# Kernel tuning notes

Measured on AMD Instinct MI355X. Metric: run time of the kernel, lower is better.

Reference implementation:

```python
import jax, jax.numpy as jnp
import numpy as np

DIM = 180
HEADS = 6
HEAD_DIM = DIM // HEADS
SCALE = HEAD_DIM ** (-0.5)
BW, N, K = 8192, 64, 16


def setup_inputs() -> dict:
    key = jax.random.key(0)
    ks = jax.random.split(key, 6)
    return {
        "x": jax.random.normal(ks[0], (BW, N, DIM), dtype=jnp.float32),
        "bpe_windows": jax.random.normal(ks[1], (BW, N, K), dtype=jnp.float32),
        "qkv_w": jax.random.normal(ks[2], (3 * DIM, DIM), dtype=jnp.float32) * 0.05,
        "qkv_b": jax.random.normal(ks[3], (3 * DIM,), dtype=jnp.float32) * 0.05,
        "proj_w": jax.random.normal(ks[4], (DIM, DIM), dtype=jnp.float32) * 0.05,
        "proj_b": jax.random.normal(ks[5], (DIM,), dtype=jnp.float32) * 0.05,
        "tau": jnp.ones((HEADS, 1, 1), dtype=jnp.float32),
    }


def reference(x, bpe_windows, qkv_w, qkv_b, proj_w, proj_b, tau):
    B_, n, C = x.shape
    # qkv projection -> (3, B_, H, N, hd)
    qkv = (x @ qkv_w.T + qkv_b).reshape(B_, n, 3, HEADS, HEAD_DIM)
    qkv = jnp.transpose(qkv, (2, 0, 3, 1, 4))
    q, k, v = qkv[0], qkv[1], qkv[2]
    q = q * SCALE
    attn = jnp.einsum("bhid,bhjd->bhij", q, k)  # (B_, H, N, N)
    # geodesic bias from BPE embeddings: d_B(i,j) = ||bpe_i - bpe_j||_2
    diff = bpe_windows[:, :, None, :] - bpe_windows[:, None, :, :]  # (B_, N, N, K)
    d_B = jnp.sqrt(jnp.sum(diff * diff, axis=-1))  # (B_, N, N)
    log_W_geo = -d_B[:, None, :, :] / jnp.clip(tau, 1e-6)[None]  # (B_, H, N, N)
    attn = jax.nn.softmax(attn + log_W_geo, axis=-1)
    out = jnp.einsum("bhij,bhjd->bhid", attn, v)  # (B_, H, N, hd)
    out = jnp.transpose(out, (0, 2, 1, 3)).reshape(B_, n, C)
    return out @ proj_w.T + proj_b
```

## Files before the change

kernel.cpp:

```cpp
#include <hip/hip_runtime.h>
#include <hip/hip_fp16.h>
#include <hip/hip_bf16.h>
#include <math.h>

typedef __attribute__((ext_vector_type(8))) short short8b;
typedef __attribute__((ext_vector_type(4))) float f32x4;
typedef __attribute__((ext_vector_type(4))) unsigned short ushort4b;

#define NWIN 8192
#define NT   512
#define SCALE 0.18257418583505536f

#define XB_P 200
#define QK_P 200
#define VT_P 72
#define DB_P 68
#define ATT_P 184

#define OFF_XB  0
#define OFF_QK  25600
#define OFF_VT  51200
#define OFF_DB  65024
#define OFF_BPE 73728
#define LDS_BYTES 78848

#define WK 192

__device__ __forceinline__ unsigned int bf2pk(float lo, float hi) {
    union { __hip_bfloat162 h; unsigned int u; } cv;
    cv.h = __float22bfloat162_rn(make_float2(lo, hi));
    return cv.u;
}
__device__ __forceinline__ unsigned short bf1(float v) {
    union { __hip_bfloat16 h; unsigned short u; } cv;
    cv.h = __float2bfloat16(v);
    return cv.u;
}

__global__ void prep_weights(const float* __restrict__ qkv_w,
                             const float* __restrict__ proj_w,
                             unsigned short* __restrict__ wqr,
                             unsigned short* __restrict__ wpr)
{
    const int idx = blockIdx.x * 256 + threadIdx.x;
    if (idx < 540 * WK) {
        const int r = idx / WK, k = idx % WK;
        const int seg = r / 30, dd = r % 30;
        const int which = seg / 6, hh = seg % 6;
        float v = 0.f;
        if (k < 180)
            v = qkv_w[(which * 180 + hh * 30 + dd) * 180 + k];
        wqr[idx] = bf1(v);
    }
    const int j = idx - 540 * WK;
    if (j >= 0 && j < WK * WK) {
        const int r = j / WK, k = j % WK;
        float v = 0.f;
        if (r < 180 && k < 180)
            v = proj_w[r * 180 + k];
        wpr[j] = bf1(v);
    }
}

__global__ void __launch_bounds__(NT, 3)
waga_mfma(const float* __restrict__ x,
          const float* __restrict__ bpe,
          const unsigned short* __restrict__ wqr,
          const unsigned short* __restrict__ wpr,
          const float* __restrict__ qkv_b,
          const float* __restrict__ proj_b,
          const float* __restrict__ tau,
          float* __restrict__ out)
{
    extern __shared__ char smem[];
    unsigned short* xb   = (unsigned short*)(smem + OFF_XB);
    unsigned short* qk   = (unsigned short*)(smem + OFF_QK);
    unsigned short* vT   = (unsigned short*)(smem + OFF_VT);
    unsigned short* dBs  = (unsigned short*)(smem + OFF_DB);
    float*          bpes = (float*)(smem + OFF_BPE);

    const int b = blockIdx.x;
    const int t = threadIdx.x;
    const int w = t >> 6;
    const int l = t & 63;
    const int lr = l & 15;
    const int g  = l >> 4;

    unsigned short* attg = (unsigned short*)((char*)out + (size_t)b * 46080 + 22528);

    if (t < 192) {
        const int n = t / 3, c = t % 3;
        *reinterpret_cast<uint2*>(xb + n * XB_P + 180 + 4 * c) = make_uint2(0u, 0u);
    } else if (t < 256) {
        const int n = t - 192;
        ushort4b z = {0, 0, 0, 0};
        *reinterpret_cast<ushort4b*>(attg + n * ATT_P + 180) = z;
    }
    {
        const float* xw = x + (size_t)b * 11520;
        for (int i = t; i < 64 * 45; i += NT) {
            const int n = i / 45, c4 = i % 45;
            const float4 v = *reinterpret_cast<const float4*>(xw + i * 4);
            *reinterpret_cast<uint2*>(xb + n * XB_P + c4 * 4) =
                make_uint2(bf2pk(v.x, v.y), bf2pk(v.z, v.w));
        }
    }
    if (t < 256) {
        const float4 v = *reinterpret_cast<const float4*>(bpe + (size_t)b * 1024 + t * 4);
        *reinterpret_cast<float4*>(bpes + (t >> 2) * 20 + (t & 3) * 4) = v;
    }
    __syncthreads();

    {
        const int ti = t >> 4, tj = t & 15;
        float acc0[4] = {0.f, 0.f, 0.f, 0.f};
        float acc1[4] = {0.f, 0.f, 0.f, 0.f};
        #pragma unroll
        for (int k4 = 0; k4 < 4; ++k4) {
            const float4 a0 = *reinterpret_cast<const float4*>(bpes + ti * 20 + 4 * k4);
            const float4 a1 = *reinterpret_cast<const float4*>(bpes + (ti + 32) * 20 + 4 * k4);
            #pragma unroll
            for (int e = 0; e < 4; ++e) {
                const float4 bb = *reinterpret_cast<const float4*>(bpes + (tj + 16 * e) * 20 + 4 * k4);
                float d;
                d = a0.x - bb.x; acc0[e] += d * d;
                d = a0.y - bb.y; acc0[e] += d * d;
                d = a0.z - bb.z; acc0[e] += d * d;
                d = a0.w - bb.w; acc0[e] += d * d;
                d = a1.x - bb.x; acc1[e] += d * d;
                d = a1.y - bb.y; acc1[e] += d * d;
                d = a1.z - bb.z; acc1[e] += d * d;
                d = a1.w - bb.w; acc1[e] += d * d;
            }
        }
        #pragma unroll
        for (int e = 0; e < 4; ++e) {
            dBs[ti * DB_P + tj + 16 * e] =
                __half_as_ushort(__float2half_rn(sqrtf(acc0[e])));
            dBs[(ti + 32) * DB_P + tj + 16 * e] =
                __half_as_ushort(__float2half_rn(sqrtf(acc1[e])));
        }
    }

    for (int pass = 0; pass < 2; ++pass) {
        if (pass) __syncthreads();

        {
            f32x4 acc[3][4];
            const unsigned short* wrow[3];
            bool has[3], arow_ok[3];
            int whichv[3], hhl[3], halfv[3];
            #pragma unroll
            for (int ti = 0; ti < 3; ++ti) {
                const int tl = w + 8 * ti;
                has[ti] = (tl < 18);
                const int tls = has[ti] ? tl : 0;
                const int segl = tls >> 1;
                halfv[ti] = tls & 1;
                whichv[ti] = segl / 3;
                hhl[ti] = segl % 3;
                const int hg = 3 * pass + hhl[ti];
                const int wseg = whichv[ti] * 6 + hg;
                const int ddr = halfv[ti] * 16 + lr;
                arow_ok[ti] = (ddr < 30);
                wrow[ti] = wqr + (size_t)(wseg * 30 + (arow_ok[ti] ? ddr : 0)) * WK;
                const int ddb = halfv[ti] * 16 + g * 4;
                const int cbase = whichv[ti] * 180 + hg * 30;
                f32x4 binit;
                #pragma unroll
                for (int i = 0; i < 4; ++i)
                    binit[i] = (ddb + i < 30) ? qkv_b[cbase + ddb + i] : 0.f;
                #pragma unroll
                for (int mt = 0; mt < 4; ++mt) acc[ti][mt] = binit;
            }
            #pragma unroll
            for (int kk = 0; kk < 6; ++kk) {
                short8b xf[4];
                #pragma unroll
                for (int mt = 0; mt < 4; ++mt)
                    xf[mt] = *reinterpret_cast<const short8b*>(
                        xb + (mt * 16 + lr) * XB_P + kk * 32 + g * 8);
                #pragma unroll
                for (int ti = 0; ti < 3; ++ti) {
                    if (!has[ti]) continue;
                    short8b wfv;
                    if (arow_ok[ti])
                        wfv = *reinterpret_cast<const short8b*>(wrow[ti] + kk * 32 + g * 8);
                    else
                        wfv = short8b{0, 0, 0, 0, 0, 0, 0, 0};
                    #pragma unroll
                    for (int mt = 0; mt < 4; ++mt)
                        acc[ti][mt] = __builtin_amdgcn_mfma_f32_16x16x32_bf16(
                            wfv, xf[mt], acc[ti][mt], 0, 0, 0);
                }
            }
            #pragma unroll
            for (int ti = 0; ti < 3; ++ti) {
                if (!has[ti]) continue;
                const int ddb = halfv[ti] * 16 + g * 4;
                #pragma unroll
                for (int mt = 0; mt < 4; ++mt) {
                    const int tok = mt * 16 + lr;
                    float v0 = acc[ti][mt][0], v1 = acc[ti][mt][1];
                    float v2 = acc[ti][mt][2], v3 = acc[ti][mt][3];
                    if (whichv[ti] == 0) { v0 *= SCALE; v1 *= SCALE; v2 *= SCALE; v3 *= SCALE; }
                    if (whichv[ti] < 2) {
                        *reinterpret_cast<uint2*>(
                            qk + tok * QK_P + hhl[ti] * 64 + whichv[ti] * 32 + ddb) =
                            make_uint2(bf2pk(v0, v1), bf2pk(v2, v3));
                    } else {
                        const int c = (tok & 32) + ((tok >> 2) & 3) * 8 + ((tok >> 4) & 1) * 4 + (tok & 3);
                        unsigned short* vb = vT + hhl[ti] * 2304 + ddb * VT_P + c;
                        vb[0 * VT_P] = bf1(v0);
                        vb[1 * VT_P] = bf1(v1);
                        vb[2 * VT_P] = bf1(v2);
                        vb[3 * VT_P] = bf1(v3);
                    }
                }
            }
        }
        __syncthreads();

        for (int u = w; u < 12; u += 8) {
            const int hh = u >> 2, mt = u & 3;
            const int h = 3 * pass + hh;
            const int tok = mt * 16 + lr;
            const unsigned short* qkh = qk + hh * 64;
            const short8b qf = *reinterpret_cast<const short8b*>(
                qkh + tok * QK_P + g * 8);
            short8b kf[4];
            #pragma unroll
            for (int jt = 0; jt < 4; ++jt)
                kf[jt] = *reinterpret_cast<const short8b*>(
                    qkh + (jt * 16 + lr) * QK_P + 32 + g * 8);
            short8b vf[2][2];
            #pragma unroll
            for (int ntd = 0; ntd < 2; ++ntd)
                #pragma unroll
                for (int ks = 0; ks < 2; ++ks)
                    vf[ntd][ks] = *reinterpret_cast<const short8b*>(
                        vT + hh * 2304 + (ntd * 16 + lr) * VT_P + ks * 32 + g * 8);
            const float itau = 1.f / fmaxf(tau[h], 1e-6f);
            f32x4 s[4];
            #pragma unroll
            for (int jt = 0; jt < 4; ++jt) {
                const ushort4b du = *reinterpret_cast<const ushort4b*>(
                    dBs + tok * DB_P + jt * 16 + g * 4);
                #pragma unroll
                for (int i = 0; i < 4; ++i)
                    s[jt][i] = -itau * __half2float(__ushort_as_half(du[i]));
            }
            __builtin_amdgcn_s_setprio(1);
            #pragma unroll
            for (int jt = 0; jt < 4; ++jt)
                s[jt] = __builtin_amdgcn_mfma_f32_16x16x32_bf16(kf[jt], qf, s[jt], 0, 0, 0);
            __builtin_amdgcn_s_setprio(0);
            float m4[4], a4[4];
            #pragma unroll
            for (int i = 0; i < 4; ++i)
                m4[i] = fmaxf(fmaxf(s[0][i], s[1][i]), fmaxf(s[2][i], s[3][i]));
            float mx = fmaxf(fmaxf(m4[0], m4[1]), fmaxf(m4[2], m4[3]));
            mx = fmaxf(mx, __shfl_xor(mx, 16));
            mx = fmaxf(mx, __shfl_xor(mx, 32));
            #pragma unroll
            for (int jt = 0; jt < 4; ++jt)
                #pragma unroll
                for (int i = 0; i < 4; ++i)
                    s[jt][i] = __expf(s[jt][i] - mx);
            #pragma unroll
            for (int i = 0; i < 4; ++i)
                a4[i] = (s[0][i] + s[1][i]) + (s[2][i] + s[3][i]);
            float sum = (a4[0] + a4[1]) + (a4[2] + a4[3]);
            sum += __shfl_xor(sum, 16);
            sum += __shfl_xor(sum, 32);
            const float inv = 1.f / sum;
            union { short8b v; unsigned int u[4]; } pb[2];
            #pragma unroll
            for (int ks = 0; ks < 2; ++ks) {
                pb[ks].u[0] = bf2pk(s[2 * ks][0] * inv, s[2 * ks][1] * inv);
                pb[ks].u[1] = bf2pk(s[2 * ks][2] * inv, s[2 * ks][3] * inv);
                pb[ks].u[2] = bf2pk(s[2 * ks + 1][0] * inv, s[2 * ks + 1][1] * inv);
                pb[ks].u[3] = bf2pk(s[2 * ks + 1][2] * inv, s[2 * ks + 1][3] * inv);
            }
            __builtin_amdgcn_s_setprio(1);
            f32x4 o0 = {0.f, 0.f, 0.f, 0.f}, o1 = {0.f, 0.f, 0.f, 0.f};
            o0 = __builtin_amdgcn_mfma_f32_16x16x32_bf16(vf[0][0], pb[0].v, o0, 0, 0, 0);
            o1 = __builtin_amdgcn_mfma_f32_16x16x32_bf16(vf[1][0], pb[0].v, o1, 0, 0, 0);
            o0 = __builtin_amdgcn_mfma_f32_16x16x32_bf16(vf[0][1], pb[1].v, o0, 0, 0, 0);
            o1 = __builtin_amdgcn_mfma_f32_16x16x32_bf16(vf[1][1], pb[1].v, o1, 0, 0, 0);
            __builtin_amdgcn_s_setprio(0);
            {
                const int col0 = h * 30 + g * 4;
                *reinterpret_cast<uint2*>(attg + tok * ATT_P + col0) =
                    make_uint2(bf2pk(o0[0], o0[1]), bf2pk(o0[2], o0[3]));
                const int col1 = h * 30 + 16 + g * 4;
                if (g < 3) {
                    *reinterpret_cast<uint2*>(attg + tok * ATT_P + col1) =
                        make_uint2(bf2pk(o1[0], o1[1]), bf2pk(o1[2], o1[3]));
                } else {
                    *reinterpret_cast<unsigned int*>(attg + tok * ATT_P + col1) =
                        bf2pk(o1[0], o1[1]);
                }
            }
        }
    }
    __syncthreads();

    {
        const int mt = w & 3;
        const int ntb = (w >> 2) * 6;
        short8b attf[6];
        #pragma unroll
        for (int kk = 0; kk < 6; ++kk) {
            if (kk == 5 && g == 3)
                attf[kk] = short8b{0, 0, 0, 0, 0, 0, 0, 0};
            else
                attf[kk] = *reinterpret_cast<const short8b*>(
                    attg + (mt * 16 + lr) * ATT_P + kk * 32 + g * 8);
        }
        f32x4 pacc[6];
        short8b wf[6];
        #pragma unroll
        for (int kk = 0; kk < 6; ++kk)
            wf[kk] = *reinterpret_cast<const short8b*>(
                wpr + (size_t)(ntb * 16 + lr) * WK + kk * 32 + g * 8);
        #pragma unroll
        for (int q6 = 0; q6 < 6; ++q6) {
            short8b wcur[6];
            #pragma unroll
            for (int kk = 0; kk < 6; ++kk) wcur[kk] = wf[kk];
            if (q6 < 5) {
                const unsigned short* wrown =
                    wpr + (size_t)((ntb + q6 + 1) * 16 + lr) * WK;
                #pragma unroll
                for (int kk = 0; kk < 6; ++kk)
                    wf[kk] = *reinterpret_cast<const short8b*>(wrown + kk * 32 + g * 8);
            }
            const int cb = (ntb + q6) * 16 + g * 4;
            f32x4 acc;
            #pragma unroll
            for (int i = 0; i < 4; ++i)
                acc[i] = (cb + i < 180) ? proj_b[cb + i] : 0.f;
            #pragma unroll
            for (int kk = 0; kk < 6; ++kk)
                acc = __builtin_amdgcn_mfma_f32_16x16x32_bf16(wcur[kk], attf[kk], acc, 0, 0, 0);
            pacc[q6] = acc;
        }
        __syncthreads();
        #pragma unroll
        for (int q6 = 0; q6 < 6; ++q6) {
            const int cb = (ntb + q6) * 16 + g * 4;
            if (cb < 177) {
                const int tok = mt * 16 + lr;
                *reinterpret_cast<float4*>(out + ((size_t)b * 64 + tok) * 180 + cb) =
                    make_float4(pacc[q6][0], pacc[q6][1], pacc[q6][2], pacc[q6][3]);
            }
        }
    }
}

extern "C" void kernel_launch(void* const* d_in, const int* in_sizes, int n_in,
                              void* d_out, int out_size, void* d_ws, size_t ws_size,
                              hipStream_t stream) {
    (void)in_sizes; (void)n_in; (void)out_size; (void)ws_size;
    const float* x      = (const float*)d_in[0];
    const float* bpe    = (const float*)d_in[1];
    const float* qkv_w  = (const float*)d_in[2];
    const float* qkv_b  = (const float*)d_in[3];
    const float* proj_w = (const float*)d_in[4];
    const float* proj_b = (const float*)d_in[5];
    const float* tau    = (const float*)d_in[6];

    unsigned short* wqr = (unsigned short*)d_ws;
    unsigned short* wpr = wqr + 540 * WK;

    prep_weights<<<(540 * WK + WK * WK + 255) / 256, 256, 0, stream>>>(
        qkv_w, proj_w, wqr, wpr);

    (void)hipFuncSetAttribute((const void*)waga_mfma,
                              hipFuncAttributeMaxDynamicSharedMemorySize,
                              LDS_BYTES);
    waga_mfma<<<NWIN, NT, LDS_BYTES, stream>>>(x, bpe, wqr, wpr, qkv_b, proj_b, tau,
                                               (float*)d_out);
}
```

Before: 737.0 us.

## Switch QKV and output projections to 32x32x16 bf16 MFMA tiles

Rewrites the QKV projection and the output projection to use 32x32x16 bf16 MFMA instructions in place of 16x16x32 ones. Each wave now covers a 32-token by 32-channel tile, and the work is split across waves differently. The QKV bias moves into LDS and is added after accumulation instead of seeding the accumulators. The aim is fewer MFMA issues and fewer fragment loads per output element, at the cost of larger accumulator register use and a different output index mapping, which could pressure occupancy.

```diff
diff --git a/kernel.cpp b/kernel.cpp
--- a/kernel.cpp
+++ b/kernel.cpp
@@ -5,6 +5,7 @@
 
 typedef __attribute__((ext_vector_type(8))) short short8b;
 typedef __attribute__((ext_vector_type(4))) float f32x4;
+typedef __attribute__((ext_vector_type(16))) float f32x16;
 typedef __attribute__((ext_vector_type(4))) unsigned short ushort4b;
 
 #define NWIN 8192
@@ -17,12 +18,13 @@
 #define DB_P 68
 #define ATT_P 184
 
-#define OFF_XB  0
-#define OFF_QK  25600
-#define OFF_VT  51200
-#define OFF_DB  65024
-#define OFF_BPE 73728
-#define LDS_BYTES 78848
+#define OFF_XB   0
+#define OFF_QK   25600
+#define OFF_VT   51200
+#define OFF_DB   65024
+#define OFF_BPE  73728
+#define OFF_QKVB 78848
+#define LDS_BYTES 81152
 
 #define WK 192
 
@@ -78,6 +80,7 @@
     unsigned short* vT   = (unsigned short*)(smem + OFF_VT);
     unsigned short* dBs  = (unsigned short*)(smem + OFF_DB);
     float*          bpes = (float*)(smem + OFF_BPE);
+    float*          qkvb = (float*)(smem + OFF_QKVB);
 
     const int b = blockIdx.x;
     const int t = threadIdx.x;
@@ -85,6 +88,8 @@
     const int l = t & 63;
     const int lr = l & 15;
     const int g  = l >> 4;
+    const int r31 = l & 31;
+    const int h5 = l >> 5;
 
     unsigned short* attg = (unsigned short*)((char*)out + (size_t)b * 46080 + 22528);
 
@@ -108,6 +113,11 @@
     if (t < 256) {
         const float4 v = *reinterpret_cast<const float4*>(bpe + (size_t)b * 1024 + t * 4);
         *reinterpret_cast<float4*>(bpes + (t >> 2) * 20 + (t & 3) * 4) = v;
+    }
+    for (int i = t; i < 576; i += NT) {
+        const int segp = i >> 5, dd = i & 31;
+        const int which = segp / 6, hg = segp % 6;
+        qkvb[i] = (dd < 30) ? qkv_b[which * 180 + hg * 30 + dd] : 0.f;
     }
     __syncthreads();
 
@@ -146,71 +156,58 @@
         if (pass) __syncthreads();
 
         {
-            f32x4 acc[3][4];
-            const unsigned short* wrow[3];
-            bool has[3], arow_ok[3];
-            int whichv[3], hhl[3], halfv[3];
-            #pragma unroll
-            for (int ti = 0; ti < 3; ++ti) {
-                const int tl = w + 8 * ti;
-                has[ti] = (tl < 18);
-                const int tls = has[ti] ? tl : 0;
-                const int segl = tls >> 1;
-                halfv[ti] = tls & 1;
-                whichv[ti] = segl / 3;
-                hhl[ti] = segl % 3;
-                const int hg = 3 * pass + hhl[ti];
-                const int wseg = whichv[ti] * 6 + hg;
-                const int ddr = halfv[ti] * 16 + lr;
-                arow_ok[ti] = (ddr < 30);
-                wrow[ti] = wqr + (size_t)(wseg * 30 + (arow_ok[ti] ? ddr : 0)) * WK;
-                const int ddb = halfv[ti] * 16 + g * 4;
-                const int cbase = whichv[ti] * 180 + hg * 30;
-                f32x4 binit;
-                #pragma unroll
-                for (int i = 0; i < 4; ++i)
-                    binit[i] = (ddb + i < 30) ? qkv_b[cbase + ddb + i] : 0.f;
-                #pragma unroll
-                for (int mt = 0; mt < 4; ++mt) acc[ti][mt] = binit;
-            }
-            #pragma unroll
-            for (int kk = 0; kk < 6; ++kk) {
-                short8b xf[4];
-                #pragma unroll
-                for (int mt = 0; mt < 4; ++mt)
-                    xf[mt] = *reinterpret_cast<const short8b*>(
-                        xb + (mt * 16 + lr) * XB_P + kk * 32 + g * 8);
-                #pragma unroll
-                for (int ti = 0; ti < 3; ++ti) {
-                    if (!has[ti]) continue;
-                    short8b wfv;
-                    if (arow_ok[ti])
-                        wfv = *reinterpret_cast<const short8b*>(wrow[ti] + kk * 32 + g * 8);
-                    else
-                        wfv = short8b{0, 0, 0, 0, 0, 0, 0, 0};
-                    #pragma unroll
-                    for (int mt = 0; mt < 4; ++mt)
-                        acc[ti][mt] = __builtin_amdgcn_mfma_f32_16x16x32_bf16(
-                            wfv, xf[mt], acc[ti][mt], 0, 0, 0);
+            const int tt = w & 1;
+            const bool has2 = (w < 2);
+            const bool aok = (r31 < 30);
+            const unsigned short* xrow = xb + (tt * 32 + r31) * XB_P;
+            int segp[3], which_[3], hh_[3];
+            const unsigned short* arow[3];
+            #pragma unroll
+            for (int i = 0; i < 3; ++i) {
+                const int tl = (w + 8 * i < 18) ? (w + 8 * i) : w;
+                const int seg = tl >> 1;
+                which_[i] = seg / 3; hh_[i] = seg % 3;
+                segp[i] = which_[i] * 6 + 3 * pass + hh_[i];
+                arow[i] = wqr + (size_t)(segp[i] * 30 + (aok ? r31 : 0)) * WK;
+            }
+            f32x16 acc[3];
+            #pragma unroll
+            for (int i = 0; i < 3; ++i)
+                #pragma unroll
+                for (int j = 0; j < 16; ++j) acc[i][j] = 0.f;
+            const short8b zf = {0, 0, 0, 0, 0, 0, 0, 0};
+            #pragma unroll
+            for (int kk = 0; kk < 12; ++kk) {
+                const short8b bfv = *reinterpret_cast<const short8b*>(xrow + kk * 16 + h5 * 8);
+                const short8b a0 = aok ? *reinterpret_cast<const short8b*>(arow[0] + kk * 16 + h5 * 8) : zf;
+                acc[0] = __builtin_amdgcn_mfma_f32_32x32x16_bf16(a0, bfv, acc[0], 0, 0, 0);
+                const short8b a1 = aok ? *reinterpret_cast<const short8b*>(arow[1] + kk * 16 + h5 * 8) : zf;
+                acc[1] = __builtin_amdgcn_mfma_f32_32x32x16_bf16(a1, bfv, acc[1], 0, 0, 0);
+                if (has2) {
+                    const short8b a2 = aok ? *reinterpret_cast<const short8b*>(arow[2] + kk * 16 + h5 * 8) : zf;
+                    acc[2] = __builtin_amdgcn_mfma_f32_32x32x16_bf16(a2, bfv, acc[2], 0, 0, 0);
                 }
             }
-            #pragma unroll
-            for (int ti = 0; ti < 3; ++ti) {
-                if (!has[ti]) continue;
-                const int ddb = halfv[ti] * 16 + g * 4;
-                #pragma unroll
-                for (int mt = 0; mt < 4; ++mt) {
-                    const int tok = mt * 16 + lr;
-                    float v0 = acc[ti][mt][0], v1 = acc[ti][mt][1];
-                    float v2 = acc[ti][mt][2], v3 = acc[ti][mt][3];
-                    if (whichv[ti] == 0) { v0 *= SCALE; v1 *= SCALE; v2 *= SCALE; v3 *= SCALE; }
-                    if (whichv[ti] < 2) {
-                        *reinterpret_cast<uint2*>(
-                            qk + tok * QK_P + hhl[ti] * 64 + whichv[ti] * 32 + ddb) =
+            const int tok = tt * 32 + r31;
+            const int cperm = (tok & 32) + ((tok >> 2) & 3) * 8 + ((tok >> 4) & 1) * 4 + (tok & 3);
+            #pragma unroll
+            for (int i = 0; i < 3; ++i) {
+                if (i == 2 && !has2) continue;
+                const int wq_ = which_[i], hhv = hh_[i];
+                #pragma unroll
+                for (int q = 0; q < 4; ++q) {
+                    const int db = 8 * q + 4 * h5;
+                    const float4 bias = *reinterpret_cast<const float4*>(qkvb + segp[i] * 32 + db);
+                    float v0 = acc[i][4 * q + 0] + bias.x;
+                    float v1 = acc[i][4 * q + 1] + bias.y;
+                    float v2 = acc[i][4 * q + 2] + bias.z;
+                    float v3 = acc[i][4 * q + 3] + bias.w;
+                    if (wq_ == 0) { v0 *= SCALE; v1 *= SCALE; v2 *= SCALE; v3 *= SCALE; }
+                    if (wq_ < 2) {
+                        *reinterpret_cast<uint2*>(qk + tok * QK_P + hhv * 64 + wq_ * 32 + db) =
                             make_uint2(bf2pk(v0, v1), bf2pk(v2, v3));
                     } else {
-                        const int c = (tok & 32) + ((tok >> 2) & 3) * 8 + ((tok >> 4) & 1) * 4 + (tok & 3);
-                        unsigned short* vb = vT + hhl[ti] * 2304 + ddb * VT_P + c;
+                        unsigned short* vb = vT + hhv * 2304 + db * VT_P + cperm;
                         vb[0 * VT_P] = bf1(v0);
                         vb[1 * VT_P] = bf1(v1);
                         vb[2 * VT_P] = bf1(v2);
@@ -307,53 +304,51 @@
     __syncthreads();
 
     {
-        const int mt = w & 3;
-        const int ntb = (w >> 2) * 6;
-        short8b attf[6];
-        #pragma unroll
-        for (int kk = 0; kk < 6; ++kk) {
-            if (kk == 5 && g == 3)
-                attf[kk] = short8b{0, 0, 0, 0, 0, 0, 0, 0};
-            else
-                attf[kk] = *reinterpret_cast<const short8b*>(
-                    attg + (mt * 16 + lr) * ATT_P + kk * 32 + g * 8);
-        }
-        f32x4 pacc[6];
-        short8b wf[6];
-        #pragma unroll
-        for (int kk = 0; kk < 6; ++kk)
-            wf[kk] = *reinterpret_cast<const short8b*>(
-                wpr + (size_t)(ntb * 16 + lr) * WK + kk * 32 + g * 8);
-        #pragma unroll
-        for (int q6 = 0; q6 < 6; ++q6) {
-            short8b wcur[6];
-            #pragma unroll
-            for (int kk = 0; kk < 6; ++kk) wcur[kk] = wf[kk];
-            if (q6 < 5) {
-                const unsigned short* wrown =
-                    wpr + (size_t)((ntb + q6 + 1) * 16 + lr) * WK;
-                #pragma unroll
-                for (int kk = 0; kk < 6; ++kk)
-                    wf[kk] = *reinterpret_cast<const short8b*>(wrown + kk * 32 + g * 8);
-            }
-            const int cb = (ntb + q6) * 16 + g * 4;
-            f32x4 acc;
-            #pragma unroll
-            for (int i = 0; i < 4; ++i)
-                acc[i] = (cb + i < 180) ? proj_b[cb + i] : 0.f;
-            #pragma unroll
-            for (int kk = 0; kk < 6; ++kk)
-                acc = __builtin_amdgcn_mfma_f32_16x16x32_bf16(wcur[kk], attf[kk], acc, 0, 0, 0);
-            pacc[q6] = acc;
+        const int tt = w & 1;
+        const int tc0 = w >> 1;
+        const int tc1 = tc0 + 4;
+        const bool has1 = (w < 4);
+        const unsigned short* brow = attg + (tt * 32 + r31) * ATT_P;
+        f32x16 pa0, pa1;
+        #pragma unroll
+        for (int j = 0; j < 16; ++j) { pa0[j] = 0.f; pa1[j] = 0.f; }
+        const short8b zf = {0, 0, 0, 0, 0, 0, 0, 0};
+        #pragma unroll
+        for (int kk = 0; kk < 12; ++kk) {
+            const short8b bfv = (kk == 11 && h5 == 1) ? zf :
+                *reinterpret_cast<const short8b*>(brow + kk * 16 + h5 * 8);
+            const short8b a0 = *reinterpret_cast<const short8b*>(
+                wpr + (size_t)(tc0 * 32 + r31) * WK + kk * 16 + h5 * 8);
+            pa0 = __builtin_amdgcn_mfma_f32_32x32x16_bf16(a0, bfv, pa0, 0, 0, 0);
+            if (has1) {
+                const short8b a1 = *reinterpret_cast<const short8b*>(
+                    wpr + (size_t)(tc1 * 32 + r31) * WK + kk * 16 + h5 * 8);
+                pa1 = __builtin_amdgcn_mfma_f32_32x32x16_bf16(a1, bfv, pa1, 0, 0, 0);
+            }
         }
         __syncthreads();
-        #pragma unroll
-        for (int q6 = 0; q6 < 6; ++q6) {
-            const int cb = (ntb + q6) * 16 + g * 4;
-            if (cb < 177) {
-                const int tok = mt * 16 + lr;
-                *reinterpret_cast<float4*>(out + ((size_t)b * 64 + tok) * 180 + cb) =
-                    make_float4(pacc[q6][0], pacc[q6][1], pacc[q6][2], pacc[q6][3]);
+        const int tok = tt * 32 + r31;
+        float* orow = out + ((size_t)b * 64 + tok) * 180;
+        #pragma unroll
+        for (int q = 0; q < 4; ++q) {
+            const int cb = tc0 * 32 + 8 * q + 4 * h5;
+            if (cb <= 176) {
+                const float4 pbv = *reinterpret_cast<const float4*>(proj_b + cb);
+                *reinterpret_cast<float4*>(orow + cb) = make_float4(
+                    pa0[4 * q + 0] + pbv.x, pa0[4 * q + 1] + pbv.y,
+                    pa0[4 * q + 2] + pbv.z, pa0[4 * q + 3] + pbv.w);
+            }
+        }
+        if (has1) {
+            #pragma unroll
+            for (int q = 0; q < 4; ++q) {
+                const int cb = tc1 * 32 + 8 * q + 4 * h5;
+                if (cb <= 176) {
+                    const float4 pbv = *reinterpret_cast<const float4*>(proj_b + cb);
+                    *reinterpret_cast<float4*>(orow + cb) = make_float4(
+                        pa1[4 * q + 0] + pbv.x, pa1[4 * q + 1] + pbv.y,
+                        pa1[4 * q + 2] + pbv.z, pa1[4 * q + 3] + pbv.w);
+                }
             }
         }
     }
```

After: 897.1 us. 1.22x slower.

## Software-pipeline per-head QKV projection with attention using double-buffered LDS

Applied to the files above, without the earlier changes.

Replaces the two-pass, three-heads-at-a-time schedule with a per-head pipeline. Warps 0-5 compute the QKV projection for head h+1 into one of two small LDS buffers while warps 4-7 run attention for head h from the other buffer. The smaller LDS footprint allows raising launch bounds to 4 blocks per CU to increase occupancy. Costs are more barriers (one per head), overlapping warp roles (warps 4-5 do both tasks), and loss of the s_setprio hints.

```diff
diff --git a/kernel.cpp b/kernel.cpp
--- a/kernel.cpp
+++ b/kernel.cpp
@@ -12,17 +12,19 @@
 #define SCALE 0.18257418583505536f
 
 #define XB_P 200
-#define QK_P 200
+#define QKB_P 72
 #define VT_P 72
 #define DB_P 68
 #define ATT_P 184
+#define QKB_SZ (64 * QKB_P)
+#define VTB_SZ (32 * VT_P)
 
 #define OFF_XB  0
-#define OFF_QK  25600
-#define OFF_VT  51200
-#define OFF_DB  65024
-#define OFF_BPE 73728
-#define LDS_BYTES 78848
+#define OFF_QKB 25600
+#define OFF_VTB 44032
+#define OFF_DB  53248
+#define OFF_BPE 61952
+#define LDS_BYTES 67072
 
 #define WK 192
 
@@ -62,7 +64,7 @@
     }
 }
 
-__global__ void __launch_bounds__(NT, 3)
+__global__ void __launch_bounds__(NT, 4)
 waga_mfma(const float* __restrict__ x,
           const float* __restrict__ bpe,
           const unsigned short* __restrict__ wqr,
@@ -73,11 +75,11 @@
           float* __restrict__ out)
 {
     extern __shared__ char smem[];
-    unsigned short* xb   = (unsigned short*)(smem + OFF_XB);
-    unsigned short* qk   = (unsigned short*)(smem + OFF_QK);
-    unsigned short* vT   = (unsigned short*)(smem + OFF_VT);
-    unsigned short* dBs  = (unsigned short*)(smem + OFF_DB);
-    float*          bpes = (float*)(smem + OFF_BPE);
+    unsigned short* xb    = (unsigned short*)(smem + OFF_XB);
+    unsigned short* qkbuf = (unsigned short*)(smem + OFF_QKB);
+    unsigned short* vTbuf = (unsigned short*)(smem + OFF_VTB);
+    unsigned short* dBs   = (unsigned short*)(smem + OFF_DB);
+    float*          bpes  = (float*)(smem + OFF_BPE);
 
     const int b = blockIdx.x;
     const int t = threadIdx.x;
@@ -142,169 +144,141 @@
         }
     }
 
-    for (int pass = 0; pass < 2; ++pass) {
-        if (pass) __syncthreads();
-
+    auto qkv_head = [&](int hg, int bufp) {
+        if (w >= 6) return;
+        const int which = w >> 1, half = w & 1;
+        const int ddr = half * 16 + lr;
+        const bool aok = (ddr < 30);
+        const unsigned short* wrow =
+            wqr + (size_t)((which * 6 + hg) * 30 + (aok ? ddr : 0)) * WK;
+        const short8b zf = {0, 0, 0, 0, 0, 0, 0, 0};
+        short8b wf[6];
+        #pragma unroll
+        for (int kk = 0; kk < 6; ++kk)
+            wf[kk] = aok ? *reinterpret_cast<const short8b*>(wrow + kk * 32 + g * 8) : zf;
+        const int ddb = half * 16 + g * 4;
+        const int cbase = which * 180 + hg * 30;
+        f32x4 binit;
+        #pragma unroll
+        for (int i = 0; i < 4; ++i)
+            binit[i] = (ddb + i < 30) ? qkv_b[cbase + ddb + i] : 0.f;
+        f32x4 acc[4] = {binit, binit, binit, binit};
+        #pragma unroll
+        for (int kk = 0; kk < 6; ++kk) {
+            #pragma unroll
+            for (int mt = 0; mt < 4; ++mt) {
+                const short8b xf = *reinterpret_cast<const short8b*>(
+                    xb + (mt * 16 + lr) * XB_P + kk * 32 + g * 8);
+                acc[mt] = __builtin_amdgcn_mfma_f32_16x16x32_bf16(wf[kk], xf, acc[mt], 0, 0, 0);
+            }
+        }
+        unsigned short* qkb = qkbuf + bufp * QKB_SZ;
+        unsigned short* vtb = vTbuf + bufp * VTB_SZ;
+        #pragma unroll
+        for (int mt = 0; mt < 4; ++mt) {
+            const int tok = mt * 16 + lr;
+            float v0 = acc[mt][0], v1 = acc[mt][1], v2 = acc[mt][2], v3 = acc[mt][3];
+            if (which == 0) { v0 *= SCALE; v1 *= SCALE; v2 *= SCALE; v3 *= SCALE; }
+            if (which < 2) {
+                *reinterpret_cast<uint2*>(qkb + tok * QKB_P + which * 32 + ddb) =
+                    make_uint2(bf2pk(v0, v1), bf2pk(v2, v3));
+            } else {
+                const int c = (tok & 32) + ((tok >> 2) & 3) * 8 + ((tok >> 4) & 1) * 4 + (tok & 3);
+                unsigned short* vb = vtb + ddb * VT_P + c;
+                vb[0 * VT_P] = bf1(v0);
+                vb[1 * VT_P] = bf1(v1);
+                vb[2 * VT_P] = bf1(v2);
+                vb[3 * VT_P] = bf1(v3);
+            }
+        }
+    };
+
+    auto attn_head = [&](int h, int bufp) {
+        if (w < 4) return;
+        const int mt = w - 4;
+        const int tok = mt * 16 + lr;
+        const unsigned short* qkb = qkbuf + bufp * QKB_SZ;
+        const unsigned short* vtb = vTbuf + bufp * VTB_SZ;
+        const short8b qf = *reinterpret_cast<const short8b*>(qkb + tok * QKB_P + g * 8);
+        short8b kf[4];
+        #pragma unroll
+        for (int jt = 0; jt < 4; ++jt)
+            kf[jt] = *reinterpret_cast<const short8b*>(
+                qkb + (jt * 16 + lr) * QKB_P + 32 + g * 8);
+        short8b vf[2][2];
+        #pragma unroll
+        for (int ntd = 0; ntd < 2; ++ntd)
+            #pragma unroll
+            for (int ks = 0; ks < 2; ++ks)
+                vf[ntd][ks] = *reinterpret_cast<const short8b*>(
+                    vtb + (ntd * 16 + lr) * VT_P + ks * 32 + g * 8);
+        const float itau = 1.f / fmaxf(tau[h], 1e-6f);
+        f32x4 s[4];
+        #pragma unroll
+        for (int jt = 0; jt < 4; ++jt) {
+            const ushort4b du = *reinterpret_cast<const ushort4b*>(
+                dBs + tok * DB_P + jt * 16 + g * 4);
+            #pragma unroll
+            for (int i = 0; i < 4; ++i)
+                s[jt][i] = -itau * __half2float(__ushort_as_half(du[i]));
+        }
+        #pragma unroll
+        for (int jt = 0; jt < 4; ++jt)
+            s[jt] = __builtin_amdgcn_mfma_f32_16x16x32_bf16(kf[jt], qf, s[jt], 0, 0, 0);
+        float m4[4], a4[4];
+        #pragma unroll
+        for (int i = 0; i < 4; ++i)
+            m4[i] = fmaxf(fmaxf(s[0][i], s[1][i]), fmaxf(s[2][i], s[3][i]));
+        float mx = fmaxf(fmaxf(m4[0], m4[1]), fmaxf(m4[2], m4[3]));
+        mx = fmaxf(mx, __shfl_xor(mx, 16));
+        mx = fmaxf(mx, __shfl_xor(mx, 32));
+        #pragma unroll
+        for (int jt = 0; jt < 4; ++jt)
+            #pragma unroll
+            for (int i = 0; i < 4; ++i)
+                s[jt][i] = __expf(s[jt][i] - mx);
+        #pragma unroll
+        for (int i = 0; i < 4; ++i)
+            a4[i] = (s[0][i] + s[1][i]) + (s[2][i] + s[3][i]);
+        float sum = (a4[0] + a4[1]) + (a4[2] + a4[3]);
+        sum += __shfl_xor(sum, 16);
+        sum += __shfl_xor(sum, 32);
+        const float inv = 1.f / sum;
+        union { short8b v; unsigned int u[4]; } pb[2];
+        #pragma unroll
+        for (int ks = 0; ks < 2; ++ks) {
+            pb[ks].u[0] = bf2pk(s[2 * ks][0] * inv, s[2 * ks][1] * inv);
+            pb[ks].u[1] = bf2pk(s[2 * ks][2] * inv, s[2 * ks][3] * inv);
+            pb[ks].u[2] = bf2pk(s[2 * ks + 1][0] * inv, s[2 * ks + 1][1] * inv);
+            pb[ks].u[3] = bf2pk(s[2 * ks + 1][2] * inv, s[2 * ks + 1][3] * inv);
+        }
+        f32x4 o0 = {0.f, 0.f, 0.f, 0.f}, o1 = {0.f, 0.f, 0.f, 0.f};
+        o0 = __builtin_amdgcn_mfma_f32_16x16x32_bf16(vf[0][0], pb[0].v, o0, 0, 0, 0);
+        o1 = __builtin_amdgcn_mfma_f32_16x16x32_bf16(vf[1][0], pb[0].v, o1, 0, 0, 0);
+        o0 = __builtin_amdgcn_mfma_f32_16x16x32_bf16(vf[0][1], pb[1].v, o0, 0, 0, 0);
+        o1 = __builtin_amdgcn_mfma_f32_16x16x32_bf16(vf[1][1], pb[1].v, o1, 0, 0, 0);
         {
-            f32x4 acc[3][4];
-            const unsigned short* wrow[3];
-            bool has[3], arow_ok[3];
-            int whichv[3], hhl[3], halfv[3];
-            #pragma unroll
-            for (int ti = 0; ti < 3; ++ti) {
-                const int tl = w + 8 * ti;
-                has[ti] = (tl < 18);
-                const int tls = has[ti] ? tl : 0;
-                const int segl = tls >> 1;
-                halfv[ti] = tls & 1;
-                whichv[ti] = segl / 3;
-                hhl[ti] = segl % 3;
-                const int hg = 3 * pass + hhl[ti];
-                const int wseg = whichv[ti] * 6 + hg;
-                const int ddr = halfv[ti] * 16 + lr;
-                arow_ok[ti] = (ddr < 30);
-                wrow[ti] = wqr + (size_t)(wseg * 30 + (arow_ok[ti] ? ddr : 0)) * WK;
-                const int ddb = halfv[ti] * 16 + g * 4;
-                const int cbase = whichv[ti] * 180 + hg * 30;
-                f32x4 binit;
-                #pragma unroll
-                for (int i = 0; i < 4; ++i)
-                    binit[i] = (ddb + i < 30) ? qkv_b[cbase + ddb + i] : 0.f;
-                #pragma unroll
-                for (int mt = 0; mt < 4; ++mt) acc[ti][mt] = binit;
-            }
-            #pragma unroll
-            for (int kk = 0; kk < 6; ++kk) {
-                short8b xf[4];
-                #pragma unroll
-                for (int mt = 0; mt < 4; ++mt)
-                    xf[mt] = *reinterpret_cast<const short8b*>(
-                        xb + (mt * 16 + lr) * XB_P + kk * 32 + g * 8);
-                #pragma unroll
-                for (int ti = 0; ti < 3; ++ti) {
-                    if (!has[ti]) continue;
-                    short8b wfv;
-                    if (arow_ok[ti])
-                        wfv = *reinterpret_cast<const short8b*>(wrow[ti] + kk * 32 + g * 8);
-                    else
-                        wfv = short8b{0, 0, 0, 0, 0, 0, 0, 0};
-                    #pragma unroll
-                    for (int mt = 0; mt < 4; ++mt)
-                        acc[ti][mt] = __builtin_amdgcn_mfma_f32_16x16x32_bf16(
-                            wfv, xf[mt], acc[ti][mt], 0, 0, 0);
-                }
-            }
-            #pragma unroll
-            for (int ti = 0; ti < 3; ++ti) {
-                if (!has[ti]) continue;
-                const int ddb = halfv[ti] * 16 + g * 4;
-                #pragma unroll
-                for (int mt = 0; mt < 4; ++mt) {
-                    const int tok = mt * 16 + lr;
-                    float v0 = acc[ti][mt][0], v1 = acc[ti][mt][1];
-                    float v2 = acc[ti][mt][2], v3 = acc[ti][mt][3];
-                    if (whichv[ti] == 0) { v0 *= SCALE; v1 *= SCALE; v2 *= SCALE; v3 *= SCALE; }
-                    if (whichv[ti] < 2) {
-                        *reinterpret_cast<uint2*>(
-                            qk + tok * QK_P + hhl[ti] * 64 + whichv[ti] * 32 + ddb) =
-                            make_uint2(bf2pk(v0, v1), bf2pk(v2, v3));
-                    } else {
-                        const int c = (tok & 32) + ((tok >> 2) & 3) * 8 + ((tok >> 4) & 1) * 4 + (tok & 3);
-                        unsigned short* vb = vT + hhl[ti] * 2304 + ddb * VT_P + c;
-                        vb[0 * VT_P] = bf1(v0);
-                        vb[1 * VT_P] = bf1(v1);
-                        vb[2 * VT_P] = bf1(v2);
-                        vb[3 * VT_P] = bf1(v3);
-                    }
-                }
-            }
-        }
+            const int col0 = h * 30 + g * 4;
+            *reinterpret_cast<uint2*>(attg + tok * ATT_P + col0) =
+                make_uint2(bf2pk(o0[0], o0[1]), bf2pk(o0[2], o0[3]));
+            const int col1 = h * 30 + 16 + g * 4;
+            if (g < 3) {
+                *reinterpret_cast<uint2*>(attg + tok * ATT_P + col1) =
+                    make_uint2(bf2pk(o1[0], o1[1]), bf2pk(o1[2], o1[3]));
+            } else {
+                *reinterpret_cast<unsigned int*>(attg + tok * ATT_P + col1) =
+                    bf2pk(o1[0], o1[1]);
+            }
+        }
+    };
+
+    qkv_head(0, 0);
+    __syncthreads();
+    for (int h = 0; h < 6; ++h) {
+        if (h < 5) qkv_head(h + 1, (h + 1) & 1);
+        attn_head(h, h & 1);
         __syncthreads();
-
-        for (int u = w; u < 12; u += 8) {
-            const int hh = u >> 2, mt = u & 3;
-            const int h = 3 * pass + hh;
-            const int tok = mt * 16 + lr;
-            const unsigned short* qkh = qk + hh * 64;
-            const short8b qf = *reinterpret_cast<const short8b*>(
-                qkh + tok * QK_P + g * 8);
-            short8b kf[4];
-            #pragma unroll
-            for (int jt = 0; jt < 4; ++jt)
-                kf[jt] = *reinterpret_cast<const short8b*>(
-                    qkh + (jt * 16 + lr) * QK_P + 32 + g * 8);
-            short8b vf[2][2];
-            #pragma unroll
-            for (int ntd = 0; ntd < 2; ++ntd)
-                #pragma unroll
-                for (int ks = 0; ks < 2; ++ks)
-                    vf[ntd][ks] = *reinterpret_cast<const short8b*>(
-                        vT + hh * 2304 + (ntd * 16 + lr) * VT_P + ks * 32 + g * 8);
-            const float itau = 1.f / fmaxf(tau[h], 1e-6f);
-            f32x4 s[4];
-            #pragma unroll
-            for (int jt = 0; jt < 4; ++jt) {
-                const ushort4b du = *reinterpret_cast<const ushort4b*>(
-                    dBs + tok * DB_P + jt * 16 + g * 4);
-                #pragma unroll
-                for (int i = 0; i < 4; ++i)
-                    s[jt][i] = -itau * __half2float(__ushort_as_half(du[i]));
-            }
-            __builtin_amdgcn_s_setprio(1);
-            #pragma unroll
-            for (int jt = 0; jt < 4; ++jt)
-                s[jt] = __builtin_amdgcn_mfma_f32_16x16x32_bf16(kf[jt], qf, s[jt], 0, 0, 0);
-            __builtin_amdgcn_s_setprio(0);
-            float m4[4], a4[4];
-            #pragma unroll
-            for (int i = 0; i < 4; ++i)
-                m4[i] = fmaxf(fmaxf(s[0][i], s[1][i]), fmaxf(s[2][i], s[3][i]));
-            float mx = fmaxf(fmaxf(m4[0], m4[1]), fmaxf(m4[2], m4[3]));
-            mx = fmaxf(mx, __shfl_xor(mx, 16));
-            mx = fmaxf(mx, __shfl_xor(mx, 32));
-            #pragma unroll
-            for (int jt = 0; jt < 4; ++jt)
-                #pragma unroll
-                for (int i = 0; i < 4; ++i)
-                    s[jt][i] = __expf(s[jt][i] - mx);
-            #pragma unroll
-            for (int i = 0; i < 4; ++i)
-                a4[i] = (s[0][i] + s[1][i]) + (s[2][i] + s[3][i]);
-            float sum = (a4[0] + a4[1]) + (a4[2] + a4[3]);
-            sum += __shfl_xor(sum, 16);
-            sum += __shfl_xor(sum, 32);
-            const float inv = 1.f / sum;
-            union { short8b v; unsigned int u[4]; } pb[2];
-            #pragma unroll
-            for (int ks = 0; ks < 2; ++ks) {
-                pb[ks].u[0] = bf2pk(s[2 * ks][0] * inv, s[2 * ks][1] * inv);
-                pb[ks].u[1] = bf2pk(s[2 * ks][2] * inv, s[2 * ks][3] * inv);
-                pb[ks].u[2] = bf2pk(s[2 * ks + 1][0] * inv, s[2 * ks + 1][1] * inv);
-                pb[ks].u[3] = bf2pk(s[2 * ks + 1][2] * inv, s[2 * ks + 1][3] * inv);
-            }
-            __builtin_amdgcn_s_setprio(1);
-            f32x4 o0 = {0.f, 0.f, 0.f, 0.f}, o1 = {0.f, 0.f, 0.f, 0.f};
-            o0 = __builtin_amdgcn_mfma_f32_16x16x32_bf16(vf[0][0], pb[0].v, o0, 0, 0, 0);
-            o1 = __builtin_amdgcn_mfma_f32_16x16x32_bf16(vf[1][0], pb[0].v, o1, 0, 0, 0);
-            o0 = __builtin_amdgcn_mfma_f32_16x16x32_bf16(vf[0][1], pb[1].v, o0, 0, 0, 0);
-            o1 = __builtin_amdgcn_mfma_f32_16x16x32_bf16(vf[1][1], pb[1].v, o1, 0, 0, 0);
-            __builtin_amdgcn_s_setprio(0);
-            {
-                const int col0 = h * 30 + g * 4;
-                *reinterpret_cast<uint2*>(attg + tok * ATT_P + col0) =
-                    make_uint2(bf2pk(o0[0], o0[1]), bf2pk(o0[2], o0[3]));
-                const int col1 = h * 30 + 16 + g * 4;
-                if (g < 3) {
-                    *reinterpret_cast<uint2*>(attg + tok * ATT_P + col1) =
-                        make_uint2(bf2pk(o1[0], o1[1]), bf2pk(o1[2], o1[3]));
-                } else {
-                    *reinterpret_cast<unsigned int*>(attg + tok * ATT_P + col1) =
-                        bf2pk(o1[0], o1[1]);
-                }
-            }
-        }
-    }
-    __syncthreads();
+    }
 
     {
         const int mt = w & 3;
```

New measurement: 747.7 us. About the same (+1.4%).

## Raise occupancy to 4 blocks per CU and drop register-hungry weight prefetch

Applied to the files above, without the earlier changes.

Changes launch bounds from 3 to 4 blocks per CU, forcing a tighter register budget. To fit that budget, the projection stage no longer double-buffers proj weight fragments in registers and loads each fragment just before its MFMA. It also removes the s_setprio bracketing around the attention MFMAs. The aim is more resident waves to hide latency, at the cost of exposed global-load latency in the projection loop and possible spills. LDS use (about 77 KB per block) may also cap occupancy regardless of the new bound.

```diff
diff --git a/kernel.cpp b/kernel.cpp
--- a/kernel.cpp
+++ b/kernel.cpp
@@ -62,7 +62,7 @@
     }
 }
 
-__global__ void __launch_bounds__(NT, 3)
+__global__ void __launch_bounds__(NT, 4)
 waga_mfma(const float* __restrict__ x,
           const float* __restrict__ bpe,
           const unsigned short* __restrict__ wqr,
@@ -250,11 +250,9 @@
                 for (int i = 0; i < 4; ++i)
                     s[jt][i] = -itau * __half2float(__ushort_as_half(du[i]));
             }
-            __builtin_amdgcn_s_setprio(1);
             #pragma unroll
             for (int jt = 0; jt < 4; ++jt)
                 s[jt] = __builtin_amdgcn_mfma_f32_16x16x32_bf16(kf[jt], qf, s[jt], 0, 0, 0);
-            __builtin_amdgcn_s_setprio(0);
             float m4[4], a4[4];
             #pragma unroll
             for (int i = 0; i < 4; ++i)
@@ -282,13 +280,11 @@
                 pb[ks].u[2] = bf2pk(s[2 * ks + 1][0] * inv, s[2 * ks + 1][1] * inv);
                 pb[ks].u[3] = bf2pk(s[2 * ks + 1][2] * inv, s[2 * ks + 1][3] * inv);
             }
-            __builtin_amdgcn_s_setprio(1);
             f32x4 o0 = {0.f, 0.f, 0.f, 0.f}, o1 = {0.f, 0.f, 0.f, 0.f};
             o0 = __builtin_amdgcn_mfma_f32_16x16x32_bf16(vf[0][0], pb[0].v, o0, 0, 0, 0);
             o1 = __builtin_amdgcn_mfma_f32_16x16x32_bf16(vf[1][0], pb[0].v, o1, 0, 0, 0);
             o0 = __builtin_amdgcn_mfma_f32_16x16x32_bf16(vf[0][1], pb[1].v, o0, 0, 0, 0);
             o1 = __builtin_amdgcn_mfma_f32_16x16x32_bf16(vf[1][1], pb[1].v, o1, 0, 0, 0);
-            __builtin_amdgcn_s_setprio(0);
             {
                 const int col0 = h * 30 + g * 4;
                 *reinterpret_cast<uint2*>(attg + tok * ATT_P + col0) =
@@ -319,37 +315,27 @@
                     attg + (mt * 16 + lr) * ATT_P + kk * 32 + g * 8);
         }
         f32x4 pacc[6];
-        short8b wf[6];
-        #pragma unroll
-        for (int kk = 0; kk < 6; ++kk)
-            wf[kk] = *reinterpret_cast<const short8b*>(
-                wpr + (size_t)(ntb * 16 + lr) * WK + kk * 32 + g * 8);
         #pragma unroll
         for (int q6 = 0; q6 < 6; ++q6) {
-            short8b wcur[6];
-            #pragma unroll
-            for (int kk = 0; kk < 6; ++kk) wcur[kk] = wf[kk];
-            if (q6 < 5) {
-                const unsigned short* wrown =
-                    wpr + (size_t)((ntb + q6 + 1) * 16 + lr) * WK;
-                #pragma unroll
-                for (int kk = 0; kk < 6; ++kk)
-                    wf[kk] = *reinterpret_cast<const short8b*>(wrown + kk * 32 + g * 8);
-            }
-            const int cb = (ntb + q6) * 16 + g * 4;
+            const int nt = ntb + q6;
+            const unsigned short* wrow = wpr + (size_t)(nt * 16 + lr) * WK;
+            const int cb = nt * 16 + g * 4;
             f32x4 acc;
             #pragma unroll
             for (int i = 0; i < 4; ++i)
                 acc[i] = (cb + i < 180) ? proj_b[cb + i] : 0.f;
             #pragma unroll
-            for (int kk = 0; kk < 6; ++kk)
-                acc = __builtin_amdgcn_mfma_f32_16x16x32_bf16(wcur[kk], attf[kk], acc, 0, 0, 0);
+            for (int kk = 0; kk < 6; ++kk) {
+                const short8b wf = *reinterpret_cast<const short8b*>(wrow + kk * 32 + g * 8);
+                acc = __builtin_amdgcn_mfma_f32_16x16x32_bf16(wf, attf[kk], acc, 0, 0, 0);
+            }
             pacc[q6] = acc;
         }
         __syncthreads();
         #pragma unroll
         for (int q6 = 0; q6 < 6; ++q6) {
-            const int cb = (ntb + q6) * 16 + g * 4;
+            const int nt = ntb + q6;
+            const int cb = nt * 16 + g * 4;
             if (cb < 177) {
                 const int tok = mt * 16 + lr;
                 *reinterpret_cast<float4*>(out + ((size_t)b * 64 + tok) * 180 + cb) =
```

New measurement: 724.9 us. No clear change (-1.6%).
